# Performance work log

Hardware: AMD Instinct MI355X
Metric: run time of the kernel (lower is better)

Reference implementation:

```python
import jax, jax.numpy as jnp
import numpy as np

M, D, S, K, DIN = 512, 10, 16384, 1024, 784  # test points, classes, jacobian dim, n_eigh, input dim


def setup_inputs() -> dict:
    key = jax.random.key(0)
    k0, k1, k2, k3, k4 = jax.random.split(key, 5)
    X_test = jax.random.normal(k0, (M, DIN), dtype=jnp.float32)
    Jz = jax.random.normal(k1, (M, D, S), dtype=jnp.float32) * 0.02      # backend.jacobians(X_test)
    v = jax.random.normal(k2, (S, K), dtype=jnp.float32) * 0.02          # self.v from fit()
    A = jax.random.normal(k3, (K, K), dtype=jnp.float32) * 0.02
    G_inv = 0.5 * (A + A.T) + jnp.eye(K, dtype=jnp.float32)              # symmetric, like an inverse PSD matrix
    W_net = jax.random.normal(k4, (DIN, D), dtype=jnp.float32) * 0.02    # stand-in for self.net
    return {"X_test": X_test, "Jz": Jz, "v": v, "G_inv": G_inv, "W_net": W_net}


def reference(X_test, Jz, v, G_inv, W_net):
    # phi: (d, m, k) -- per-class ELLA features of each test point
    phi = jnp.einsum('mds,sk->dmk', Jz, v)
    # Full (class, class, n, m) covariance tensor, exactly as the torch module computes it
    K_test = jnp.einsum('ank,kg,bmg->abnm', phi, G_inv, phi)
    mean = X_test @ W_net                                # self.net(X_test)
    var = jnp.diagonal(K_test, axis1=-2, axis2=-1)       # (d, d, n) -- discards off-diagonal n,m
    return mean, jnp.transpose(var, (2, 0, 1))           # (n, d, d)
```

## Files before the change

kernel.cpp:

```cpp
#include <hip/hip_runtime.h>
#include <hip/hip_bf16.h>

#define M_PTS 512
#define D_CLS 10
#define S_DIM 16384
#define K_DIM 1024
#define DIN_  784
#define PHI_ELEMS (5120 * 1024)

typedef short  bf16x8  __attribute__((ext_vector_type(8)));
typedef float  f32x4   __attribute__((ext_vector_type(4)));
typedef uint   uintx4  __attribute__((ext_vector_type(4)));
typedef ushort ushort8 __attribute__((ext_vector_type(8)));

__device__ __forceinline__ ushort f2bfu(float f) {
    __bf16 h = (__bf16)f;
    return __builtin_bit_cast(ushort, h);
}
__device__ __forceinline__ uint pkbf(float a, float b) {
    return (uint)f2bfu(a) | ((uint)f2bfu(b) << 16);
}

__global__ __launch_bounds__(64) void mean_kernel(const float* __restrict__ X,
                                                  const float* __restrict__ W,
                                                  float* __restrict__ out) {
    int m = blockIdx.x;
    int lane = threadIdx.x;
    float acc[D_CLS];
#pragma unroll
    for (int d = 0; d < D_CLS; ++d) acc[d] = 0.f;
    for (int i = lane; i < DIN_; i += 64) {
        float x = X[(size_t)m * DIN_ + i];
#pragma unroll
        for (int d = 0; d < D_CLS; ++d) acc[d] += x * W[i * D_CLS + d];
    }
#pragma unroll
    for (int d = 0; d < D_CLS; ++d) {
        float v = acc[d];
        for (int off = 32; off > 0; off >>= 1) v += __shfl_down(v, off);
        if (lane == 0) out[(size_t)m * D_CLS + d] = v;
    }
}

__global__ __launch_bounds__(256) void cvt_a(const float* __restrict__ src,
                                             ushort* __restrict__ dst, int n8) {
    for (int i = blockIdx.x * 256 + threadIdx.x; i < n8; i += gridDim.x * 256) {
        float4 a = reinterpret_cast<const float4*>(src)[2 * i];
        float4 b = reinterpret_cast<const float4*>(src)[2 * i + 1];
        ushort8 o;
        o[0] = f2bfu(a.x); o[1] = f2bfu(a.y); o[2] = f2bfu(a.z); o[3] = f2bfu(a.w);
        o[4] = f2bfu(b.x); o[5] = f2bfu(b.y); o[6] = f2bfu(b.z); o[7] = f2bfu(b.w);
        reinterpret_cast<ushort8*>(dst)[i] = o;
    }
}

__global__ __launch_bounds__(256) void cvt_bt(const float* __restrict__ v,
                                              ushort* __restrict__ bt) {
    __shared__ float tile[64][65];
    const int kt = blockIdx.x;
    const int ct = blockIdx.y;
    const int t  = threadIdx.x;
    const int col4 = t & 15, row = t >> 4;
#pragma unroll
    for (int i = 0; i < 4; ++i) {
        int r = row + 16 * i;
        float4 v4 = *reinterpret_cast<const float4*>(
            v + (size_t)(kt * 64 + r) * K_DIM + ct * 64 + col4 * 4);
        tile[r][col4 * 4 + 0] = v4.x; tile[r][col4 * 4 + 1] = v4.y;
        tile[r][col4 * 4 + 2] = v4.z; tile[r][col4 * 4 + 3] = v4.w;
    }
    __syncthreads();
#pragma unroll
    for (int i = 0; i < 2; ++i) {
        int cid = i * 256 + t;
        int c = cid >> 3, kc = cid & 7;
        ushort8 o;
#pragma unroll
        for (int j = 0; j < 8; ++j) o[j] = f2bfu(tile[kc * 8 + j][c]);
        *reinterpret_cast<ushort8*>(bt + (size_t)(ct * 64 + c) * S_DIM +
                                    kt * 64 + kc * 8) = o;
    }
}

template <int SD, int KSP>
__global__ __launch_bounds__(256, 4) void gemm_bb(const ushort* __restrict__ A,
                                                  const ushort* __restrict__ BT,
                                                  float* __restrict__ Cout) {
    __shared__ ushort As[2][4096];
    __shared__ ushort Bs[2][4096];

    const int nwg = 320 * KSP;
    const int lid = blockIdx.x;
    const int swz = (lid & 7) * (nwg >> 3) + (lid >> 3);
    const int kp  = swz / 320;
    const int rem = swz - kp * 320;
    const int bm  = rem >> 3;
    const int bn  = rem & 7;
    const int KSTEPS = SD / 32 / KSP;
    const int kbase  = kp * (SD / KSP);

    const int t  = threadIdx.x;
    const int l  = t & 63;
    const int wm = (t >> 7) & 1;
    const int wn = (t >> 6) & 1;
    const int lr = l & 15;
    const int kq = l >> 4;

    const ushort* Ablk = A  + (size_t)(bm * 128) * SD + kbase;
    const ushort* Bblk = BT + (size_t)(bn * 128) * SD + kbase;

    f32x4 acc[4][4];
#pragma unroll
    for (int i = 0; i < 4; ++i)
#pragma unroll
        for (int j = 0; j < 4; ++j) acc[i][j] = (f32x4)0.f;

#define GSTAGE(BUF, S, SRC, DST)                                                \
    { _Pragma("unroll") for (int i = 0; i < 2; ++i) {                           \
        const int cch = i * 256 + t;                                            \
        const int r = cch >> 2, sl = cch & 3;                                   \
        const ushort* gp = SRC + (size_t)r * SD + (S) * 32 +                    \
                           ((sl ^ ((r >> 1) & 3)) << 3);                        \
        ushort* lp = &DST[BUF][(i * 256 + (t & 192)) * 8];                      \
        __builtin_amdgcn_global_load_lds(                                       \
            (const __attribute__((address_space(1))) void*)gp,                  \
            (__attribute__((address_space(3))) void*)lp, 16, 0, 0);             \
      } }

#define GCOMPUTE(BUF)                                                           \
    { bf16x8 fa[4], fb[4];                                                      \
      _Pragma("unroll") for (int mi = 0; mi < 4; ++mi) {                        \
        const int r = wm * 64 + mi * 16 + lr;                                   \
        fa[mi] = *reinterpret_cast<const bf16x8*>(                              \
            &As[BUF][(r * 4 + (kq ^ ((r >> 1) & 3))) * 8]);                     \
      }                                                                         \
      _Pragma("unroll") for (int ni = 0; ni < 4; ++ni) {                        \
        const int c = wn * 64 + ni * 16 + lr;                                   \
        fb[ni] = *reinterpret_cast<const bf16x8*>(                              \
            &Bs[BUF][(c * 4 + (kq ^ ((c >> 1) & 3))) * 8]);                     \
      }                                                                         \
      _Pragma("unroll") for (int ni = 0; ni < 4; ++ni)                          \
        _Pragma("unroll") for (int mi = 0; mi < 4; ++mi)                        \
          acc[mi][ni] = __builtin_amdgcn_mfma_f32_16x16x32_bf16(                \
              fa[mi], fb[ni], acc[mi][ni], 0, 0, 0);                            \
    }

    GSTAGE(0, 0, Ablk, As)
    GSTAGE(0, 0, Bblk, Bs)
    __syncthreads();

    for (int s = 0; s < KSTEPS; ++s) {
        const int cb = s & 1, nb = cb ^ 1;
        if (s + 1 < KSTEPS) {
            GSTAGE(nb, s + 1, Ablk, As)
            GSTAGE(nb, s + 1, Bblk, Bs)
        }
        GCOMPUTE(cb)
        __syncthreads();
    }

    float* C = Cout + (size_t)kp * PHI_ELEMS;
#pragma unroll
    for (int mi = 0; mi < 4; ++mi) {
        int orow = bm * 128 + wm * 64 + mi * 16 + kq * 4;
#pragma unroll
        for (int ni = 0; ni < 4; ++ni) {
            int ocol = bn * 128 + wn * 64 + ni * 16 + lr;
            float* cp = C + (size_t)orow * K_DIM + ocol;
#pragma unroll
            for (int rr = 0; rr < 4; ++rr) cp[(size_t)rr * K_DIM] = acc[mi][ni][rr];
        }
    }
#undef GSTAGE
#undef GCOMPUTE
}

template <int KSP, bool F32OUT>
__global__ __launch_bounds__(256) void phi_reduce(float* __restrict__ phi,
                                                  ushort* __restrict__ phib) {
    const int n8 = PHI_ELEMS / 8;
    for (int i = blockIdx.x * 256 + threadIdx.x; i < n8; i += gridDim.x * 256) {
        f32x4 s0 = reinterpret_cast<f32x4*>(phi)[2 * i];
        f32x4 s1 = reinterpret_cast<f32x4*>(phi)[2 * i + 1];
#pragma unroll
        for (int p = 1; p < KSP; ++p) {
            s0 += reinterpret_cast<f32x4*>(phi + (size_t)p * PHI_ELEMS)[2 * i];
            s1 += reinterpret_cast<f32x4*>(phi + (size_t)p * PHI_ELEMS)[2 * i + 1];
        }
        if (F32OUT) {
            reinterpret_cast<f32x4*>(phi)[2 * i]     = s0;
            reinterpret_cast<f32x4*>(phi)[2 * i + 1] = s1;
        }
        ushort8 o;
        o[0] = f2bfu(s0[0]); o[1] = f2bfu(s0[1]); o[2] = f2bfu(s0[2]); o[3] = f2bfu(s0[3]);
        o[4] = f2bfu(s1[0]); o[5] = f2bfu(s1[1]); o[6] = f2bfu(s1[2]); o[7] = f2bfu(s1[3]);
        reinterpret_cast<ushort8*>(phib)[i] = o;
    }
}

__global__ __launch_bounds__(256) void var_contract(const float* __restrict__ T,
                                                    const float* __restrict__ P,
                                                    float* __restrict__ out) {
    __shared__ float red[4][56];
    const int n = blockIdx.x, t = threadIdx.x, lane = t & 63, wid = t >> 6;
    const float* Tn = T + (size_t)n * D_CLS * K_DIM;
    const float* Pn = P + (size_t)n * D_CLS * K_DIM;
    float Ta[D_CLS][4], Pb[D_CLS][4];
#pragma unroll
    for (int a = 0; a < D_CLS; ++a)
#pragma unroll
        for (int j = 0; j < 4; ++j) {
            Ta[a][j] = Tn[a * K_DIM + t + 256 * j];
            Pb[a][j] = Pn[a * K_DIM + t + 256 * j];
        }
    int p = 0;
#pragma unroll
    for (int a = 0; a < D_CLS; ++a)
#pragma unroll
        for (int b = 0; b <= a; ++b, ++p) {
            float s = Ta[a][0] * Pb[b][0] + Ta[a][1] * Pb[b][1]
                    + Ta[a][2] * Pb[b][2] + Ta[a][3] * Pb[b][3];
#pragma unroll
            for (int off = 32; off > 0; off >>= 1) s += __shfl_down(s, off);
            if (lane == 0) red[wid][p] = s;
        }
    __syncthreads();
    if (t < 55) {
        int a = 0;
        while ((a + 1) * (a + 2) / 2 <= t) ++a;
        int b = t - a * (a + 1) / 2;
        float s = red[0][t] + red[1][t] + red[2][t] + red[3][t];
        float* vout = out + M_PTS * D_CLS + (size_t)n * D_CLS * D_CLS;
        vout[a * D_CLS + b] = s;
        vout[b * D_CLS + a] = s;
    }
}

template <int SD, int KSP>
__global__ __launch_bounds__(256, 2) void gemm_f32(const float* __restrict__ A,
                                                   const float* __restrict__ B,
                                                   float* __restrict__ Cout) {
    __shared__ float As[3][4096];
    __shared__ uint  Bs[3][16 * 132];
    const int nwg = 320 * KSP;
    const int lid = blockIdx.x;
    const int swz = (lid & 7) * (nwg >> 3) + (lid >> 3);
    const int kp  = swz / 320;
    const int rem = swz - kp * 320;
    const int bm  = rem >> 3;
    const int bn  = rem & 7;
    const int KSTEPS = SD / 32 / KSP;
    const int kbase  = kp * (SD / KSP);
    const int t  = threadIdx.x;
    const int l  = t & 63;
    const int wm = (t >> 7) & 1;
    const int wn = (t >> 6) & 1;
    const int lr = l & 15;
    const int kq = l >> 4;
    const float* Ablk = A + (size_t)(bm * 128) * SD + kbase;
    const int c4 = t >> 3;
    const int kd = t & 7;
    const float* Bcol = B + (size_t)kbase * K_DIM + bn * 128 + c4 * 4;
    float bregA[2][2][4], bregB[2][2][4];
    f32x4 acc[4][4];
#pragma unroll
    for (int i = 0; i < 4; ++i)
#pragma unroll
        for (int j = 0; j < 4; ++j) acc[i][j] = (f32x4)0.f;
#define FSTAGE_A(BUF, S)                                                        \
    { _Pragma("unroll") for (int i = 0; i < 4; ++i) {                           \
        const int c = i * 256 + t;                                              \
        const int row = c >> 3, sl = c & 7;                                     \
        const float* gp = Ablk + (size_t)row * SD + (S) * 32 +                  \
                          ((sl ^ (row & 7)) << 2);                              \
        float* lp = &As[BUF][(i * 256 + (t & 192)) << 2];                       \
        __builtin_amdgcn_global_load_lds(                                       \
            (const __attribute__((address_space(1))) void*)gp,                  \
            (__attribute__((address_space(3))) void*)lp, 16, 0, 0);             \
      } }
#define FLOAD_B(RG, S)                                                          \
    { _Pragma("unroll") for (int j2 = 0; j2 < 2; ++j2)                          \
      _Pragma("unroll") for (int j = 0; j < 2; ++j) {                           \
        float4 b4 = *reinterpret_cast<const float4*>(                           \
            Bcol + (size_t)((S) * 32 + (kd + 8 * j2) * 2 + j) * K_DIM);         \
        RG[j2][j][0] = b4.x; RG[j2][j][1] = b4.y;                               \
        RG[j2][j][2] = b4.z; RG[j2][j][3] = b4.w;                               \
      } }
#define FWRITE_B(BUF, RG)                                                       \
    { _Pragma("unroll") for (int j2 = 0; j2 < 2; ++j2) {                        \
        uintx4 w;                                                               \
        w.x = pkbf(RG[j2][0][0], RG[j2][1][0]);                                 \
        w.y = pkbf(RG[j2][0][1], RG[j2][1][1]);                                 \
        w.z = pkbf(RG[j2][0][2], RG[j2][1][2]);                                 \
        w.w = pkbf(RG[j2][0][3], RG[j2][1][3]);                                 \
        *reinterpret_cast<uintx4*>(&Bs[BUF][(kd + 8 * j2) * 132 + c4 * 4]) = w; \
      } }
#define FCOMPUTE(BUF)                                                           \
    { const f32x4* Av = reinterpret_cast<const f32x4*>(&As[BUF][0]);            \
      const uint* Bv = &Bs[BUF][0];                                             \
      bf16x8 fa[4];                                                             \
      _Pragma("unroll") for (int mi = 0; mi < 4; ++mi) {                        \
        const int row = wm * 64 + mi * 16 + lr;                                 \
        f32x4 a0 = Av[row * 8 + ((kq * 2) ^ (row & 7))];                        \
        f32x4 a1 = Av[row * 8 + ((kq * 2 + 1) ^ (row & 7))];                    \
        uintx4 uu;                                                              \
        uu.x = pkbf(a0.x, a0.y); uu.y = pkbf(a0.z, a0.w);                       \
        uu.z = pkbf(a1.x, a1.y); uu.w = pkbf(a1.z, a1.w);                       \
        fa[mi] = __builtin_bit_cast(bf16x8, uu);                                \
      }                                                                         \
      _Pragma("unroll") for (int ni = 0; ni < 4; ++ni) {                        \
        const int cc = wn * 64 + ni * 16 + lr;                                  \
        uintx4 uv;                                                              \
        uv.x = Bv[(kq * 4 + 0) * 132 + cc];                                     \
        uv.y = Bv[(kq * 4 + 1) * 132 + cc];                                     \
        uv.z = Bv[(kq * 4 + 2) * 132 + cc];                                     \
        uv.w = Bv[(kq * 4 + 3) * 132 + cc];                                     \
        bf16x8 fb = __builtin_bit_cast(bf16x8, uv);                             \
        _Pragma("unroll") for (int mi = 0; mi < 4; ++mi)                        \
          acc[mi][ni] = __builtin_amdgcn_mfma_f32_16x16x32_bf16(                \
              fa[mi], fb, acc[mi][ni], 0, 0, 0);                                \
      } }
    FLOAD_B(bregA, 0)
    FSTAGE_A(0, 0)
    asm volatile("s_waitcnt vmcnt(0)" ::: "memory");
    FWRITE_B(0, bregA)
    FLOAD_B(bregB, 1)
    FSTAGE_A(1, 1)
    asm volatile("s_waitcnt lgkmcnt(0)" ::: "memory");
    __builtin_amdgcn_s_barrier();
    const int NIT = KSTEPS / 2;
    for (int s2 = 0; s2 < NIT - 1; ++s2) {
        const int s = 2 * s2;
        const int cb0 = s % 3, wb0 = (s + 1) % 3, sb0 = (s + 2) % 3;
        FLOAD_B(bregA, s + 2)
        FSTAGE_A(sb0, s + 2)
        asm volatile("" ::: "memory");
        FCOMPUTE(cb0)
        asm volatile("s_waitcnt vmcnt(8)" ::: "memory");
        FWRITE_B(wb0, bregB)
        asm volatile("s_waitcnt lgkmcnt(0)" ::: "memory");
        __builtin_amdgcn_s_barrier();
        FLOAD_B(bregB, s + 3)
        FSTAGE_A(cb0, s + 3)
        asm volatile("" ::: "memory");
        FCOMPUTE(wb0)
        asm volatile("s_waitcnt vmcnt(8)" ::: "memory");
        FWRITE_B(sb0, bregA)
        asm volatile("s_waitcnt lgkmcnt(0)" ::: "memory");
        __builtin_amdgcn_s_barrier();
    }
    {
        const int cb = (KSTEPS - 2) % 3, wb = (KSTEPS - 1) % 3;
        FCOMPUTE(cb)
        asm volatile("s_waitcnt vmcnt(0)" ::: "memory");
        FWRITE_B(wb, bregB)
        asm volatile("s_waitcnt lgkmcnt(0)" ::: "memory");
        __builtin_amdgcn_s_barrier();
        FCOMPUTE(wb)
    }
    float* C = Cout + (size_t)kp * PHI_ELEMS;
#pragma unroll
    for (int mi = 0; mi < 4; ++mi) {
        int orow = bm * 128 + wm * 64 + mi * 16 + kq * 4;
#pragma unroll
        for (int ni = 0; ni < 4; ++ni) {
            int ocol = bn * 128 + wn * 64 + ni * 16 + lr;
            float* cp = C + (size_t)orow * K_DIM + ocol;
#pragma unroll
            for (int rr = 0; rr < 4; ++rr) cp[(size_t)rr * K_DIM] = acc[mi][ni][rr];
        }
    }
#undef FSTAGE_A
#undef FLOAD_B
#undef FWRITE_B
#undef FCOMPUTE
}

template <int KSP>
__global__ __launch_bounds__(256) void phi_reduce_f32(float* __restrict__ phi) {
    const int NT = PHI_ELEMS / 4;
    for (int idx = blockIdx.x * 256 + threadIdx.x; idx < NT; idx += 256 * 2048) {
        f32x4 s = reinterpret_cast<f32x4*>(phi)[idx];
#pragma unroll
        for (int p = 1; p < KSP; ++p)
            s += reinterpret_cast<f32x4*>(phi + (size_t)p * PHI_ELEMS)[idx];
        reinterpret_cast<f32x4*>(phi)[idx] = s;
    }
}

__global__ __launch_bounds__(256) void var_kernel_valu(const float* __restrict__ phi,
                                                       const float* __restrict__ G,
                                                       float* __restrict__ out) {
    __shared__ float ph[D_CLS][K_DIM];
    __shared__ float red[4][56];
    const int n = blockIdx.x, t = threadIdx.x, lane = t & 63, wid = t >> 6;
    const size_t base = (size_t)n * D_CLS * K_DIM;
    for (int i = t; i < D_CLS * K_DIM / 4; i += 256)
        reinterpret_cast<float4*>(&ph[0][0])[i] =
            reinterpret_cast<const float4*>(phi + base)[i];
    __syncthreads();
    float Tacc[D_CLS][4];
#pragma unroll
    for (int a = 0; a < D_CLS; ++a)
#pragma unroll
        for (int j = 0; j < 4; ++j) Tacc[a][j] = 0.f;
#pragma unroll 4
    for (int k = 0; k < K_DIM; ++k) {
        const float* Grow = G + (size_t)k * K_DIM + t;
        float g0 = Grow[0], g1 = Grow[256], g2 = Grow[512], g3 = Grow[768];
#pragma unroll
        for (int a = 0; a < D_CLS; ++a) {
            float pv = ph[a][k];
            Tacc[a][0] += pv * g0; Tacc[a][1] += pv * g1;
            Tacc[a][2] += pv * g2; Tacc[a][3] += pv * g3;
        }
    }
    float pb[D_CLS][4];
#pragma unroll
    for (int b = 0; b < D_CLS; ++b)
#pragma unroll
        for (int j = 0; j < 4; ++j) pb[b][j] = ph[b][t + 256 * j];
    int p = 0;
#pragma unroll
    for (int a = 0; a < D_CLS; ++a)
#pragma unroll
        for (int b = 0; b <= a; ++b, ++p) {
            float s = Tacc[a][0] * pb[b][0] + Tacc[a][1] * pb[b][1]
                    + Tacc[a][2] * pb[b][2] + Tacc[a][3] * pb[b][3];
#pragma unroll
            for (int off = 32; off > 0; off >>= 1) s += __shfl_down(s, off);
            if (lane == 0) red[wid][p] = s;
        }
    __syncthreads();
    if (t < 55) {
        int a = 0;
        while ((a + 1) * (a + 2) / 2 <= t) ++a;
        int b = t - a * (a + 1) / 2;
        float s = red[0][t] + red[1][t] + red[2][t] + red[3][t];
        float* vout = out + M_PTS * D_CLS + (size_t)n * D_CLS * D_CLS;
        vout[a * D_CLS + b] = s;
        vout[b * D_CLS + a] = s;
    }
}

extern "C" void kernel_launch(void* const* d_in, const int* in_sizes, int n_in,
                              void* d_out, int out_size, void* d_ws, size_t ws_size,
                              hipStream_t stream) {
    const float* X  = (const float*)d_in[0];
    const float* Jz = (const float*)d_in[1];
    const float* v  = (const float*)d_in[2];
    const float* G  = (const float*)d_in[3];
    const float* W  = (const float*)d_in[4];
    float* out = (float*)d_out;
    float* ws  = (float*)d_ws;

    const size_t PB = (size_t)PHI_ELEMS * 4;
    const size_t A_B  = (size_t)5120 * S_DIM * 2;
    const size_t BT_B = (size_t)K_DIM * S_DIM * 2;
    const size_t G_B  = (size_t)K_DIM * K_DIM * 2;
    const size_t PHB  = (size_t)PHI_ELEMS * 2;
    const size_t FULL_NEED = 5 * PB + A_B + BT_B + G_B + PHB;
    const size_t MID_NEED  = 2 * PB + A_B + BT_B + G_B + PHB;

    hipLaunchKernelGGL(mean_kernel, dim3(M_PTS), dim3(64), 0, stream, X, W, out);

    if (ws_size >= MID_NEED) {
        const int KS = (ws_size >= FULL_NEED) ? 4 : 1;
        float*  phi  = ws;
        float*  T    = ws + (size_t)KS * PHI_ELEMS;
        ushort* Abf  = (ushort*)(T + PHI_ELEMS);
        ushort* vTb  = Abf + (size_t)5120 * S_DIM;
        ushort* Gb   = vTb + (size_t)K_DIM * S_DIM;
        ushort* phib = Gb + (size_t)K_DIM * K_DIM;

        hipLaunchKernelGGL(cvt_a, dim3(2048), dim3(256), 0, stream,
                           Jz, Abf, 5120 * S_DIM / 8);
        hipLaunchKernelGGL(cvt_bt, dim3(256, 16), dim3(256), 0, stream, v, vTb);
        hipLaunchKernelGGL(cvt_a, dim3(256), dim3(256), 0, stream,
                           G, Gb, K_DIM * K_DIM / 8);
        if (KS == 4) {
            hipLaunchKernelGGL((gemm_bb<S_DIM, 4>), dim3(1280), dim3(256), 0,
                               stream, Abf, vTb, phi);
            hipLaunchKernelGGL((phi_reduce<4, true>), dim3(1024), dim3(256), 0,
                               stream, phi, phib);
        } else {
            hipLaunchKernelGGL((gemm_bb<S_DIM, 1>), dim3(320), dim3(256), 0,
                               stream, Abf, vTb, phi);
            hipLaunchKernelGGL((phi_reduce<1, false>), dim3(1024), dim3(256), 0,
                               stream, phi, phib);
        }
        hipLaunchKernelGGL((gemm_bb<K_DIM, 1>), dim3(320), dim3(256), 0, stream,
                           phib, Gb, T);
        hipLaunchKernelGGL(var_contract, dim3(M_PTS), dim3(256), 0, stream,
                           T, phi, out);
        return;
    }

    float* phi = ws;
    if (ws_size >= 5 * PB) {
        float* T = phi + (size_t)4 * PHI_ELEMS;
        hipLaunchKernelGGL((gemm_f32<S_DIM, 4>), dim3(1280), dim3(256), 0, stream, Jz, v, phi);
        hipLaunchKernelGGL(phi_reduce_f32<4>, dim3(2048), dim3(256), 0, stream, phi);
        hipLaunchKernelGGL((gemm_f32<K_DIM, 1>), dim3(320), dim3(256), 0, stream, phi, G, T);
        hipLaunchKernelGGL(var_contract, dim3(M_PTS), dim3(256), 0, stream, T, phi, out);
    } else if (ws_size >= 3 * PB) {
        float* T = phi + (size_t)2 * PHI_ELEMS;
        hipLaunchKernelGGL((gemm_f32<S_DIM, 2>), dim3(640), dim3(256), 0, stream, Jz, v, phi);
        hipLaunchKernelGGL(phi_reduce_f32<2>, dim3(2048), dim3(256), 0, stream, phi);
        hipLaunchKernelGGL((gemm_f32<K_DIM, 1>), dim3(320), dim3(256), 0, stream, phi, G, T);
        hipLaunchKernelGGL(var_contract, dim3(M_PTS), dim3(256), 0, stream, T, phi, out);
    } else if (ws_size >= 2 * PB) {
        float* T = phi + (size_t)PHI_ELEMS;
        hipLaunchKernelGGL((gemm_f32<S_DIM, 1>), dim3(320), dim3(256), 0, stream, Jz, v, phi);
        hipLaunchKernelGGL((gemm_f32<K_DIM, 1>), dim3(320), dim3(256), 0, stream, phi, G, T);
        hipLaunchKernelGGL(var_contract, dim3(M_PTS), dim3(256), 0, stream, T, phi, out);
    } else {
        hipLaunchKernelGGL((gemm_f32<S_DIM, 1>), dim3(320), dim3(256), 0, stream, Jz, v, phi);
        hipLaunchKernelGGL(var_kernel_valu, dim3(M_PTS), dim3(256), 0, stream, phi, G, out);
    }
}
```

Before: 433.3 us.

## Triple-buffer GEMM LDS staging with counted vmcnt waits and priority boost

The bf16 GEMM moves from double to triple buffering of LDS tiles, so loads for step s+2 are issued while step s computes. A full __syncthreads is replaced by a partial s_waitcnt vmcnt(4) plus a raw s_barrier, so the next tile's loads can stay in flight. MFMA compute is wrapped in s_setprio. In exchange, LDS use grows by half and occupancy drops to 3 waves per SIMD. Correctness relies on GSTAGE issuing exactly 4 vector loads per stage, and on direct-to-LDS loads being covered by vmcnt.

```diff
diff --git a/kernel.cpp b/kernel.cpp
--- a/kernel.cpp
+++ b/kernel.cpp
@@ -83,11 +83,11 @@
 }
 
 template <int SD, int KSP>
-__global__ __launch_bounds__(256, 4) void gemm_bb(const ushort* __restrict__ A,
+__global__ __launch_bounds__(256, 3) void gemm_bb(const ushort* __restrict__ A,
                                                   const ushort* __restrict__ BT,
                                                   float* __restrict__ Cout) {
-    __shared__ ushort As[2][4096];
-    __shared__ ushort Bs[2][4096];
+    __shared__ ushort As[3][4096];
+    __shared__ ushort Bs[3][4096];
 
     const int nwg = 320 * KSP;
     const int lid = blockIdx.x;
@@ -147,16 +147,33 @@
 
     GSTAGE(0, 0, Ablk, As)
     GSTAGE(0, 0, Bblk, Bs)
-    __syncthreads();
-
-    for (int s = 0; s < KSTEPS; ++s) {
-        const int cb = s & 1, nb = cb ^ 1;
-        if (s + 1 < KSTEPS) {
-            GSTAGE(nb, s + 1, Ablk, As)
-            GSTAGE(nb, s + 1, Bblk, Bs)
-        }
+    GSTAGE(1, 1, Ablk, As)
+    GSTAGE(1, 1, Bblk, Bs)
+    asm volatile("s_waitcnt vmcnt(4)" ::: "memory");
+    __builtin_amdgcn_s_barrier();
+    __builtin_amdgcn_sched_barrier(0);
+
+    for (int s = 0; s < KSTEPS - 2; ++s) {
+        const int sb = (s + 2) % 3, cb = s % 3;
+        GSTAGE(sb, s + 2, Ablk, As)
+        GSTAGE(sb, s + 2, Bblk, Bs)
+        __builtin_amdgcn_s_setprio(1);
         GCOMPUTE(cb)
-        __syncthreads();
+        __builtin_amdgcn_s_setprio(0);
+        __builtin_amdgcn_sched_barrier(0);
+        asm volatile("s_waitcnt vmcnt(4)" ::: "memory");
+        __builtin_amdgcn_s_barrier();
+        __builtin_amdgcn_sched_barrier(0);
+    }
+    {
+        __builtin_amdgcn_s_setprio(1);
+        GCOMPUTE((KSTEPS - 2) % 3)
+        __builtin_amdgcn_s_setprio(0);
+        __builtin_amdgcn_sched_barrier(0);
+        asm volatile("s_waitcnt vmcnt(0)" ::: "memory");
+        __builtin_amdgcn_s_barrier();
+        __builtin_amdgcn_sched_barrier(0);
+        GCOMPUTE((KSTEPS - 1) % 3)
     }
 
     float* C = Cout + (size_t)kp * PHI_ELEMS;
```

Result: no change. 430.4 us (-0.7%).
